# Kernel optimization log

Measured on AMD Instinct MI355X. Metric: run time of the kernel, lower is better.

The kernel has to match this reference:

```python
import jax, jax.numpy as jnp
from jax import lax
import numpy as np

ALPHA = 0.82
MAXITER = 10
N1_NODES = 2048
N2_NODES = 2048
K_ATTR = 64
EDGE_P = 0.004  # sparse-ish adjacency density


def setup_inputs() -> dict:
    key = jax.random.key(0)
    k1, k2, k3, k4 = jax.random.split(key, 4)
    A1 = (jax.random.uniform(k1, (N1_NODES, N1_NODES)) < EDGE_P).astype(jnp.float32)
    A1 = jnp.maximum(A1, A1.T)  # undirected 0/1 adjacency
    A2 = (jax.random.uniform(k2, (N2_NODES, N2_NODES)) < EDGE_P).astype(jnp.float32)
    A2 = jnp.maximum(A2, A2.T)
    N1 = jax.random.uniform(k3, (N1_NODES, K_ATTR), dtype=jnp.float32)
    N2 = jax.random.uniform(k4, (N2_NODES, K_ATTR), dtype=jnp.float32)
    # default prior (_get_H with path=None), normalized so sum ~= 1
    H = jnp.full((N2_NODES, N1_NODES), 1.0 / (N1_NODES * N2_NODES), dtype=jnp.float32)
    return {"A1": A1, "A2": A2, "N1": N1, "N2": N2, "H": H}


def _row_l2_normalize(N):
    nrm = jnp.sqrt(jnp.sum(N * N, axis=1, keepdims=True))
    return jnp.where(nrm > 0, N / jnp.where(nrm > 0, nrm, 1.0), 0.0)


def _final_forward(A1, A2, N1, N2, H, alpha=ALPHA, maxiter=MAXITER):
    # No edge attrs: L=1, E1=A1, E2=A2. T = 1/A^2 where A^2>0 (elementwise),
    # E <- E*T, so B = (E*A) = A*T*A.
    def masked_recip_sq(A):
        A2e = A * A
        return jnp.where(A2e > 0, 1.0 / jnp.where(A2e > 0, A2e, 1.0), 0.0)

    B1 = (A1 * masked_recip_sq(A1)) * A1  # (n1, n1)
    B2 = (A2 * masked_recip_sq(A2)) * A2  # (n2, n2)

    N1n = _row_l2_normalize(N1)  # (n1, K)
    N2n = _row_l2_normalize(N2)  # (n2, K)

    # Kronecker vectors laid out as (n1, n2) matrices (C-order == kron order):
    # N[i*n2+j] = sum_k N1[i,k]*N2[j,k]  -> N1n @ N2n.T
    Nm = N1n @ N2n.T  # (n1, n2)
    dm = (B1 @ N1n) @ (B2 @ N2n).T  # (n1, n2)
    D = Nm * dm
    DD = jnp.where(D > 0, lax.rsqrt(jnp.where(D > 0, D, 1.0)), 0.0)  # inf -> 0
    q = DD * Nm  # (n1, n2)

    # h = H.flatten('F') with H (n2,n1): as an (n1,n2) matrix this is H.T
    h = H.T  # (n1, n2)

    def step(s, _):
        # M = (q*s) reshaped (n2,n1) F-order == (q*s).T in our layout.
        # S = B2 @ M @ B1 (n2,n1); S.flatten('F') as (n1,n2) == B1.T @ (q*s) @ B2.T
        S_t = B1.T @ (q * s) @ B2.T  # (n1, n2)
        s_new = (1.0 - alpha) * h + alpha * q * S_t
        return s_new, None

    s, _ = lax.scan(step, h, None, length=maxiter)
    # original: s.reshape((n1, n2)) C-order -> exactly our layout
    return s  # (n1, n2) alignment matrix


def reference(A1, A2, N1, N2, H):
    return _final_forward(A1, A2, N1, N2, H)
```

## Files before the change

kernel.cpp:

```cpp
#include <hip/hip_runtime.h>

#define NMAT 2048
#define KATTR 64
#define CAP 64
#define NITER 10
#define SENT_A 2048
#define SENT_B 2057

typedef unsigned short ushort4v __attribute__((ext_vector_type(4)));

__device__ __forceinline__ unsigned short f2bf(float f) {
  unsigned u = __float_as_uint(f);
  return (unsigned short)((u + 0x7fff + ((u >> 16) & 1)) >> 16);
}
__device__ __forceinline__ float bf2f(unsigned short b) {
  return __uint_as_float((unsigned)b << 16);
}
__device__ __forceinline__ float bflo(unsigned v) {
  return __uint_as_float(v << 16);
}
__device__ __forceinline__ float bfhi(unsigned v) {
  return __uint_as_float(v & 0xffff0000u);
}
__device__ __forceinline__ int swz(int c) { return 4 * c + (((c >> 3) & 7) << 2); }

__global__ __launch_bounds__(256) void k_build2(
    const float* __restrict__ A1, const float* __restrict__ A2,
    unsigned short* __restrict__ idx1, unsigned short* __restrict__ idx2,
    unsigned short* __restrict__ idxT4, int* __restrict__ cnt1,
    int* __restrict__ cnt2) {
  __shared__ int wsum[4];
  int b = blockIdx.x;
  const float* A;
  unsigned short* idx;
  unsigned short* idxT;
  int* cnt;
  int r;
  if (b < NMAT) {
    A = A1; idx = idx1; idxT = nullptr; cnt = cnt1; r = b;
  } else {
    A = A2; idx = idx2; idxT = idxT4; cnt = cnt2; r = b - NMAT;
  }
  const float* row = A + (size_t)r * NMAT;
  int t = threadIdx.x;
  unsigned mask = 0;
  int ln = 0;
#pragma unroll
  for (int u = 0; u < 8; ++u) {
    int c = t * 8 + u;
    if (row[c] != 0.0f) {
      mask |= 1u << u;
      ++ln;
    }
  }
  int lane = t & 63, wv = t >> 6;
  int v = ln;
  for (int o = 1; o < 64; o <<= 1) {
    int x = __shfl_up(v, o);
    if (lane >= o) v += x;
  }
  if (lane == 63) wsum[wv] = v;
  __syncthreads();
  int base = 0, stot = 0;
#pragma unroll
  for (int w = 0; w < 4; ++w) {
    int x = wsum[w];
    if (w < wv) base += x;
    stot += x;
  }
  int off = base + v - ln;
#pragma unroll
  for (int u = 0; u < 8; ++u) {
    if (mask & (1u << u)) {
      int c = t * 8 + u;
      if (off < CAP) {
        idx[r * CAP + off] = (unsigned short)c;
        if (idxT)
          idxT[(size_t)(off >> 2) * (NMAT * 4) + r * 4 + (off & 3)] =
              (unsigned short)c;
      }
      ++off;
    }
  }
  int n = stot < CAP ? stot : CAP;
  for (int p = n + t; p < CAP; p += 256) {
    idx[r * CAP + p] = (unsigned short)SENT_A;
    if (idxT)
      idxT[(size_t)(p >> 2) * (NMAT * 4) + r * 4 + (p & 3)] =
          (unsigned short)SENT_B;
  }
  if (t == 0) cnt[r] = n;
}

__global__ __launch_bounds__(256) void k_norm2(const float* __restrict__ N1,
                                               const float* __restrict__ N2,
                                               float* __restrict__ N1n,
                                               float* __restrict__ N2n) {
  int half = blockIdx.x >= (NMAT / 4);
  const float* Nin = half ? N2 : N1;
  float* Nout = half ? N2n : N1n;
  int bb = half ? blockIdx.x - NMAT / 4 : blockIdx.x;
  int row = bb * 4 + (threadIdx.x >> 6);
  int lane = threadIdx.x & 63;
  float v = Nin[(size_t)row * KATTR + lane];
  float ss = v * v;
#pragma unroll
  for (int o = 32; o > 0; o >>= 1) ss += __shfl_xor(ss, o);
  float nrm = sqrtf(ss);
  Nout[(size_t)row * KATTR + lane] = (nrm > 0.f) ? v / nrm : 0.f;
}

__global__ void k_gatherN2(const unsigned short* __restrict__ idx1,
                           const int* __restrict__ cnt1,
                           const float* __restrict__ N1n,
                           float* __restrict__ C1,
                           const unsigned short* __restrict__ idx2,
                           const int* __restrict__ cnt2,
                           const float* __restrict__ N2n,
                           float* __restrict__ C2) {
  int half = blockIdx.x >= NMAT;
  const unsigned short* idx = half ? idx2 : idx1;
  const int* cnt = half ? cnt2 : cnt1;
  const float* Nn = half ? N2n : N1n;
  float* C = half ? C2 : C1;
  int i = half ? blockIdx.x - NMAT : blockIdx.x;
  int lane = threadIdx.x;
  int nn = cnt[i];
  const unsigned short* ip = idx + i * CAP;
  float acc = 0.f;
  for (int t = 0; t < nn; ++t) {
    int k = ip[t];
    acc += Nn[(size_t)k * KATTR + lane];
  }
  C[(size_t)i * KATTR + lane] = acc;
}

__global__ __launch_bounds__(1024) void k_zrow(unsigned short* __restrict__ Mb0,
                                               unsigned short* __restrict__ Mb1,
                                               float* __restrict__ Mf) {
  size_t Z = (size_t)NMAT * NMAT;
  for (int o = threadIdx.x; o < NMAT; o += 1024) {
    Mb0[Z + o] = 0;
    Mb1[Z + o] = 0;
    Mf[Z + o] = 0.f;
  }
}

__global__ __launch_bounds__(256) void k_q(
    const float* __restrict__ N1n, const float* __restrict__ C1,
    const float* __restrict__ N2n, const float* __restrict__ C2,
    const float* __restrict__ H, float* __restrict__ q,
    unsigned* __restrict__ QM, unsigned short* __restrict__ M,
    float* __restrict__ Ht) {
  __shared__ float sA[64][68];
  __shared__ float sB[64][68];
  int i0 = blockIdx.y * 64, j0 = blockIdx.x * 64;
  int c = threadIdx.x & 63, r0 = threadIdx.x >> 6;
  int tx = threadIdx.x & 15, ty = threadIdx.x >> 4;
  const float alpha = 0.82f;

  float nmv[4][4] = {};
  float dmv[4][4] = {};

  for (int r = r0; r < 64; r += 4) {
    sA[c][r] = N1n[(size_t)(i0 + r) * KATTR + c];
    sB[c][r] = N2n[(size_t)(j0 + r) * KATTR + c];
  }
  __syncthreads();
#pragma unroll 4
  for (int k = 0; k < 64; ++k) {
    float4 a = *(const float4*)&sA[k][ty * 4];
    float4 b = *(const float4*)&sB[k][tx * 4];
    float av[4] = {a.x, a.y, a.z, a.w};
    float bv[4] = {b.x, b.y, b.z, b.w};
#pragma unroll
    for (int ii = 0; ii < 4; ++ii)
#pragma unroll
      for (int jj = 0; jj < 4; ++jj)
        nmv[ii][jj] = fmaf(av[ii], bv[jj], nmv[ii][jj]);
  }
  __syncthreads();
  for (int r = r0; r < 64; r += 4) {
    sA[c][r] = C1[(size_t)(i0 + r) * KATTR + c];
    sB[c][r] = C2[(size_t)(j0 + r) * KATTR + c];
  }
  __syncthreads();
#pragma unroll 4
  for (int k = 0; k < 64; ++k) {
    float4 a = *(const float4*)&sA[k][ty * 4];
    float4 b = *(const float4*)&sB[k][tx * 4];
    float av[4] = {a.x, a.y, a.z, a.w};
    float bv[4] = {b.x, b.y, b.z, b.w};
#pragma unroll
    for (int ii = 0; ii < 4; ++ii)
#pragma unroll
      for (int jj = 0; jj < 4; ++jj)
        dmv[ii][jj] = fmaf(av[ii], bv[jj], dmv[ii][jj]);
  }
  __syncthreads();
  for (int r = r0; r < 64; r += 4)
    sA[c][r] = H[(size_t)(j0 + r) * NMAT + i0 + c];
  __syncthreads();

#pragma unroll
  for (int ii = 0; ii < 4; ++ii) {
    int i = i0 + ty * 4 + ii;
    size_t base = (size_t)i * NMAT + j0 + tx * 4;
    float4 hv = *(const float4*)&sA[ty * 4 + ii][tx * 4];
    float hvv[4] = {hv.x, hv.y, hv.z, hv.w};
    float qv[4];
    unsigned qmv[4];
    ushort4v mv;
#pragma unroll
    for (int jj = 0; jj < 4; ++jj) {
      float nmx = nmv[ii][jj];
      float D = nmx * dmv[ii][jj];
      float qq = (D > 0.f) ? nmx * rsqrtf(D) : 0.f;
      qv[jj] = qq;
      float m0 = qq * hvv[jj];
      mv[jj] = f2bf(m0);
      qmv[jj] = (unsigned)f2bf(alpha * qq * qq) |
                ((unsigned)f2bf((1.0f - alpha) * m0) << 16);
    }
    *(float4*)&q[base] = make_float4(qv[0], qv[1], qv[2], qv[3]);
    *(uint4*)&QM[base] = make_uint4(qmv[0], qmv[1], qmv[2], qmv[3]);
    *(ushort4v*)&M[base] = mv;
    *(float4*)&Ht[base] = hv;
  }
}

__global__ __launch_bounds__(1024, 8) void k_iter(
    const unsigned short* __restrict__ idx1, const int* __restrict__ cnt1,
    const unsigned short* __restrict__ idx2T4, const int* __restrict__ cnt2,
    const unsigned short* __restrict__ Min, const float* __restrict__ MinF,
    const unsigned* __restrict__ QM, const float* __restrict__ q,
    const float* __restrict__ Ht, unsigned short* __restrict__ Mout,
    float* __restrict__ MoutF, float* __restrict__ sout, int in32, int out32,
    int last) {
  __shared__ float lds[4 * NMAT + 64];
  const int GS = NMAT * 4;
  int i0 = blockIdx.x * 4;
  int tid = threadIdx.x;
  int c0 = tid * 2;

  if (tid == 0) *(float4*)&lds[swz(SENT_B)] = make_float4(0.f, 0.f, 0.f, 0.f);

  float acc[4][2];
#pragma unroll
  for (int r = 0; r < 4; ++r) {
    int nn = cnt1[i0 + r];
    const unsigned short* ip = idx1 + (i0 + r) * CAP;
    uint4 pA = *(const uint4*)(ip);
    uint4 pB = *(const uint4*)(ip + 8);
    uint4 pC = *(const uint4*)(ip + 16);
    uint4 pD = *(const uint4*)(ip + 24);
    float a0 = 0.f, a1 = 0.f;
    if (in32) {
      const float* Bf = MinF + c0;
      auto g8f = [&](uint4 pk, float2* w) {
        w[0] = *(const float2*)(Bf + (size_t)(pk.x & 0xffff) * NMAT);
        w[1] = *(const float2*)(Bf + (size_t)(pk.x >> 16) * NMAT);
        w[2] = *(const float2*)(Bf + (size_t)(pk.y & 0xffff) * NMAT);
        w[3] = *(const float2*)(Bf + (size_t)(pk.y >> 16) * NMAT);
        w[4] = *(const float2*)(Bf + (size_t)(pk.z & 0xffff) * NMAT);
        w[5] = *(const float2*)(Bf + (size_t)(pk.z >> 16) * NMAT);
        w[6] = *(const float2*)(Bf + (size_t)(pk.w & 0xffff) * NMAT);
        w[7] = *(const float2*)(Bf + (size_t)(pk.w >> 16) * NMAT);
      };
      float2 w[16];
      g8f(pA, w);
      g8f(pB, w + 8);
#pragma unroll
      for (int e = 0; e < 16; ++e) {
        a0 += w[e].x;
        a1 += w[e].y;
      }
      if (nn > 16) {
        float2 w2[16];
        g8f(pC, w2);
        g8f(pD, w2 + 8);
#pragma unroll
        for (int e = 0; e < 16; ++e) {
          a0 += w2[e].x;
          a1 += w2[e].y;
        }
      }
      for (int t = 32; t < nn; t += 8) {
        uint4 pk = *(const uint4*)(ip + t);
        float2 w3[8];
        g8f(pk, w3);
#pragma unroll
        for (int e = 0; e < 8; ++e) {
          a0 += w3[e].x;
          a1 += w3[e].y;
        }
      }
    } else {
      const unsigned short* Bb = Min + c0;
      auto g8 = [&](uint4 pk, unsigned* w) {
        w[0] = *(const unsigned*)(Bb + (size_t)(pk.x & 0xffff) * NMAT);
        w[1] = *(const unsigned*)(Bb + (size_t)(pk.x >> 16) * NMAT);
        w[2] = *(const unsigned*)(Bb + (size_t)(pk.y & 0xffff) * NMAT);
        w[3] = *(const unsigned*)(Bb + (size_t)(pk.y >> 16) * NMAT);
        w[4] = *(const unsigned*)(Bb + (size_t)(pk.z & 0xffff) * NMAT);
        w[5] = *(const unsigned*)(Bb + (size_t)(pk.z >> 16) * NMAT);
        w[6] = *(const unsigned*)(Bb + (size_t)(pk.w & 0xffff) * NMAT);
        w[7] = *(const unsigned*)(Bb + (size_t)(pk.w >> 16) * NMAT);
      };
      unsigned w[16];
      g8(pA, w);
      g8(pB, w + 8);
      bool more = nn > 16;
      unsigned w2[16];
      if (more) {
        g8(pC, w2);
        g8(pD, w2 + 8);
      }
#pragma unroll
      for (int e = 0; e < 16; ++e) {
        a0 += bflo(w[e]);
        a1 += bfhi(w[e]);
      }
      if (more) {
#pragma unroll
        for (int e = 0; e < 16; ++e) {
          a0 += bflo(w2[e]);
          a1 += bfhi(w2[e]);
        }
      }
      for (int t = 32; t < nn; t += 8) {
        uint4 pk = *(const uint4*)(ip + t);
        unsigned w3[8];
        g8(pk, w3);
#pragma unroll
        for (int e = 0; e < 8; ++e) {
          a0 += bflo(w3[e]);
          a1 += bfhi(w3[e]);
        }
      }
    }
    acc[r][0] = a0;
    acc[r][1] = a1;
  }
  *(float4*)&lds[swz(c0)] =
      make_float4(acc[0][0], acc[1][0], acc[2][0], acc[3][0]);
  *(float4*)&lds[swz(c0 + 1)] =
      make_float4(acc[0][1], acc[1][1], acc[2][1], acc[3][1]);
  __syncthreads();

  const float alpha = 0.82f;
  const float oma = 1.0f - alpha;
#pragma unroll
  for (int jj = 0; jj < 2; ++jj) {
    int j = jj * 1024 + tid;
    int nn = cnt2[j];
    const unsigned short* bp = idx2T4 + j * 4;
    size_t off0 = (size_t)i0 * NMAT + j;
    unsigned wq0 = 0, wq1 = 0, wq2 = 0, wq3 = 0;
    if (!last) {
      wq0 = QM[off0];
      wq1 = QM[off0 + NMAT];
      wq2 = QM[off0 + 2 * NMAT];
      wq3 = QM[off0 + 3 * NMAT];
    }
    uint2 g0 = *(const uint2*)(bp);
    uint2 g1 = *(const uint2*)(bp + GS);
    uint2 g2 = *(const uint2*)(bp + 2 * GS);
    uint2 g3 = *(const uint2*)(bp + 3 * GS);
    float s0 = 0.f, s1 = 0.f, s2 = 0.f, s3 = 0.f;
    float u0 = 0.f, u1 = 0.f, u2 = 0.f, u3 = 0.f;
    {
      float4 va = *(const float4*)&lds[swz(g0.x & 0xffff)];
      float4 vb = *(const float4*)&lds[swz(g0.x >> 16)];
      float4 vc = *(const float4*)&lds[swz(g0.y & 0xffff)];
      float4 vd = *(const float4*)&lds[swz(g0.y >> 16)];
      float4 ve = *(const float4*)&lds[swz(g1.x & 0xffff)];
      float4 vf = *(const float4*)&lds[swz(g1.x >> 16)];
      float4 vg = *(const float4*)&lds[swz(g1.y & 0xffff)];
      float4 vh = *(const float4*)&lds[swz(g1.y >> 16)];
      s0 += (va.x + vb.x) + (vc.x + vd.x);
      s1 += (va.y + vb.y) + (vc.y + vd.y);
      s2 += (va.z + vb.z) + (vc.z + vd.z);
      s3 += (va.w + vb.w) + (vc.w + vd.w);
      u0 += (ve.x + vf.x) + (vg.x + vh.x);
      u1 += (ve.y + vf.y) + (vg.y + vh.y);
      u2 += (ve.z + vf.z) + (vg.z + vh.z);
      u3 += (ve.w + vf.w) + (vg.w + vh.w);
    }
    {
      float4 va = *(const float4*)&lds[swz(g2.x & 0xffff)];
      float4 vb = *(const float4*)&lds[swz(g2.x >> 16)];
      float4 vc = *(const float4*)&lds[swz(g2.y & 0xffff)];
      float4 vd = *(const float4*)&lds[swz(g2.y >> 16)];
      float4 ve = *(const float4*)&lds[swz(g3.x & 0xffff)];
      float4 vf = *(const float4*)&lds[swz(g3.x >> 16)];
      float4 vg = *(const float4*)&lds[swz(g3.y & 0xffff)];
      float4 vh = *(const float4*)&lds[swz(g3.y >> 16)];
      s0 += (va.x + vb.x) + (vc.x + vd.x);
      s1 += (va.y + vb.y) + (vc.y + vd.y);
      s2 += (va.z + vb.z) + (vc.z + vd.z);
      s3 += (va.w + vb.w) + (vc.w + vd.w);
      u0 += (ve.x + vf.x) + (vg.x + vh.x);
      u1 += (ve.y + vf.y) + (vg.y + vh.y);
      u2 += (ve.z + vf.z) + (vg.z + vh.z);
      u3 += (ve.w + vf.w) + (vg.w + vh.w);
    }
    for (int t = 16; t < nn; t += 8) {
      uint2 ga = *(const uint2*)(bp + (size_t)(t >> 2) * GS);
      uint2 gb = *(const uint2*)(bp + (size_t)((t >> 2) + 1) * GS);
      float4 va = *(const float4*)&lds[swz(ga.x & 0xffff)];
      float4 vb = *(const float4*)&lds[swz(ga.x >> 16)];
      float4 vc = *(const float4*)&lds[swz(ga.y & 0xffff)];
      float4 vd = *(const float4*)&lds[swz(ga.y >> 16)];
      float4 ve = *(const float4*)&lds[swz(gb.x & 0xffff)];
      float4 vf = *(const float4*)&lds[swz(gb.x >> 16)];
      float4 vg = *(const float4*)&lds[swz(gb.y & 0xffff)];
      float4 vh = *(const float4*)&lds[swz(gb.y >> 16)];
      s0 += (va.x + vb.x) + (vc.x + vd.x);
      s1 += (va.y + vb.y) + (vc.y + vd.y);
      s2 += (va.z + vb.z) + (vc.z + vd.z);
      s3 += (va.w + vb.w) + (vc.w + vd.w);
      u0 += (ve.x + vf.x) + (vg.x + vh.x);
      u1 += (ve.y + vf.y) + (vg.y + vh.y);
      u2 += (ve.z + vf.z) + (vg.z + vh.z);
      u3 += (ve.w + vf.w) + (vg.w + vh.w);
    }
    float sa[4] = {s0 + u0, s1 + u1, s2 + u2, s3 + u3};
    if (last) {
#pragma unroll
      for (int r = 0; r < 4; ++r) {
        size_t off = off0 + (size_t)r * NMAT;
        sout[off] = oma * Ht[off] + alpha * q[off] * sa[r];
      }
    } else if (out32) {
      MoutF[off0] = fmaf(bflo(wq0), sa[0], bfhi(wq0));
      MoutF[off0 + NMAT] = fmaf(bflo(wq1), sa[1], bfhi(wq1));
      MoutF[off0 + 2 * NMAT] = fmaf(bflo(wq2), sa[2], bfhi(wq2));
      MoutF[off0 + 3 * NMAT] = fmaf(bflo(wq3), sa[3], bfhi(wq3));
    } else {
      Mout[off0] = f2bf(fmaf(bflo(wq0), sa[0], bfhi(wq0)));
      Mout[off0 + NMAT] = f2bf(fmaf(bflo(wq1), sa[1], bfhi(wq1)));
      Mout[off0 + 2 * NMAT] = f2bf(fmaf(bflo(wq2), sa[2], bfhi(wq2)));
      Mout[off0 + 3 * NMAT] = f2bf(fmaf(bflo(wq3), sa[3], bfhi(wq3)));
    }
  }
}

extern "C" void kernel_launch(void* const* d_in, const int* in_sizes, int n_in,
                              void* d_out, int out_size, void* d_ws,
                              size_t ws_size, hipStream_t stream) {
  const float* A1 = (const float*)d_in[0];
  const float* A2 = (const float*)d_in[1];
  const float* N1 = (const float*)d_in[2];
  const float* N2 = (const float*)d_in[3];
  const float* H = (const float*)d_in[4];
  float* s_out = (float*)d_out;

  char* p = (char*)d_ws;
  auto take = [&](size_t bytes) {
    char* r = p;
    p += (bytes + 255) & ~(size_t)255;
    return r;
  };
  unsigned short* idx1 = (unsigned short*)take((size_t)NMAT * CAP * 2);
  unsigned short* idx2 = (unsigned short*)take((size_t)NMAT * CAP * 2);
  unsigned short* idx2T4 = (unsigned short*)take((size_t)CAP * NMAT * 2);
  int* cnt1 = (int*)take((size_t)NMAT * 4);
  int* cnt2 = (int*)take((size_t)NMAT * 4);
  float* N1n = (float*)take((size_t)NMAT * KATTR * 4);
  float* N2n = (float*)take((size_t)NMAT * KATTR * 4);
  float* C1 = (float*)take((size_t)NMAT * KATTR * 4);
  float* C2 = (float*)take((size_t)NMAT * KATTR * 4);
  float* Ht = (float*)take((size_t)NMAT * NMAT * 4);
  float* q = (float*)take((size_t)NMAT * NMAT * 4);
  unsigned* QM = (unsigned*)take((size_t)NMAT * NMAT * 4);
  unsigned short* Mb0 = (unsigned short*)take((size_t)(NMAT + 1) * NMAT * 2);
  unsigned short* Mb1 = (unsigned short*)take((size_t)(NMAT + 1) * NMAT * 2);
  float* Mf = (float*)take((size_t)(NMAT + 1) * NMAT * 4);
  if ((size_t)(p - (char*)d_ws) > ws_size) return;

  k_build2<<<2 * NMAT, 256, 0, stream>>>(A1, A2, idx1, idx2, idx2T4, cnt1,
                                         cnt2);
  k_norm2<<<2 * (NMAT / 4), 256, 0, stream>>>(N1, N2, N1n, N2n);
  k_gatherN2<<<2 * NMAT, 64, 0, stream>>>(idx1, cnt1, N1n, C1, idx2, cnt2,
                                          N2n, C2);
  k_q<<<dim3(32, 32), 256, 0, stream>>>(N1n, C1, N2n, C2, H, q, QM, Mb0, Ht);
  k_zrow<<<1, 1024, 0, stream>>>(Mb0, Mb1, Mf);
  for (int it = 0; it < NITER; ++it) {
    const unsigned short* Min = (it & 1) ? Mb1 : Mb0;
    unsigned short* Mout = (it & 1) ? Mb0 : Mb1;
    int in32 = (it == NITER - 1) ? 1 : 0;
    int out32 = (it == NITER - 2) ? 1 : 0;
    int last = (it == NITER - 1) ? 1 : 0;
    k_iter<<<NMAT / 4, 1024, 0, stream>>>(idx1, cnt1, idx2T4, cnt2, Min, Mf,
                                          QM, q, Ht, Mout, Mf, s_out, in32,
                                          out32, last);
  }
}
```

Measured before the change: 401.8 us.

## Split iteration kernel into separate B1 and B2 sparse-product phases via fp32 intermediate

Each iteration's fused kernel is split into two launches. Phase A computes the B1 sparse gather for 32-row tiles and 256-column chunks, which gives better cache locality for the gathered rows, and writes the result to a new fp32 scratch matrix. Phase B reloads it into LDS and applies the B2 sparse product and update. This trades the fused on-chip handoff for an extra 16 MB write and read per iteration plus one more launch, in exchange for better reuse in the gather phase.

```diff
diff --git a/kernel.cpp b/kernel.cpp
--- a/kernel.cpp
+++ b/kernel.cpp
@@ -229,34 +229,30 @@
   }
 }
 
-__global__ __launch_bounds__(1024, 8) void k_iter(
+__global__ __launch_bounds__(1024, 8) void k_phA(
     const unsigned short* __restrict__ idx1, const int* __restrict__ cnt1,
-    const unsigned short* __restrict__ idx2T4, const int* __restrict__ cnt2,
     const unsigned short* __restrict__ Min, const float* __restrict__ MinF,
-    const unsigned* __restrict__ QM, const float* __restrict__ q,
-    const float* __restrict__ Ht, unsigned short* __restrict__ Mout,
-    float* __restrict__ MoutF, float* __restrict__ sout, int in32, int out32,
-    int last) {
-  __shared__ float lds[4 * NMAT + 64];
-  const int GS = NMAT * 4;
-  int i0 = blockIdx.x * 4;
+    float* __restrict__ T1, int in32) {
+  int b = blockIdx.x;
+  int chunk = b & 7, tile = b >> 3;
   int tid = threadIdx.x;
-  int c0 = tid * 2;
-
-  if (tid == 0) *(float4*)&lds[swz(SENT_B)] = make_float4(0.f, 0.f, 0.f, 0.f);
-
-  float acc[4][2];
-#pragma unroll
-  for (int r = 0; r < 4; ++r) {
-    int nn = cnt1[i0 + r];
-    const unsigned short* ip = idx1 + (i0 + r) * CAP;
+  int rg = tid >> 7;
+  int l = tid & 127;
+  int jbase = chunk * 256 + l * 2;
+  int irow0 = tile * 32 + rg * 4;
+
+#pragma unroll
+  for (int rr = 0; rr < 4; ++rr) {
+    int i = irow0 + rr;
+    int nn = cnt1[i];
+    const unsigned short* ip = idx1 + i * CAP;
     uint4 pA = *(const uint4*)(ip);
     uint4 pB = *(const uint4*)(ip + 8);
     uint4 pC = *(const uint4*)(ip + 16);
     uint4 pD = *(const uint4*)(ip + 24);
     float a0 = 0.f, a1 = 0.f;
     if (in32) {
-      const float* Bf = MinF + c0;
+      const float* Bf = MinF + jbase;
       auto g8f = [&](uint4 pk, float2* w) {
         w[0] = *(const float2*)(Bf + (size_t)(pk.x & 0xffff) * NMAT);
         w[1] = *(const float2*)(Bf + (size_t)(pk.x >> 16) * NMAT);
@@ -296,7 +292,7 @@
         }
       }
     } else {
-      const unsigned short* Bb = Min + c0;
+      const unsigned short* Bb = Min + jbase;
       auto g8 = [&](uint4 pk, unsigned* w) {
         w[0] = *(const unsigned*)(Bb + (size_t)(pk.x & 0xffff) * NMAT);
         w[1] = *(const unsigned*)(Bb + (size_t)(pk.x >> 16) * NMAT);
@@ -339,13 +335,32 @@
         }
       }
     }
-    acc[r][0] = a0;
-    acc[r][1] = a1;
-  }
-  *(float4*)&lds[swz(c0)] =
-      make_float4(acc[0][0], acc[1][0], acc[2][0], acc[3][0]);
-  *(float4*)&lds[swz(c0 + 1)] =
-      make_float4(acc[0][1], acc[1][1], acc[2][1], acc[3][1]);
+    size_t o = (size_t)i * NMAT + jbase;
+    __builtin_nontemporal_store(a0, T1 + o);
+    __builtin_nontemporal_store(a1, T1 + o + 1);
+  }
+}
+
+__global__ __launch_bounds__(1024, 8) void k_phB(
+    const unsigned short* __restrict__ idx2T4, const int* __restrict__ cnt2,
+    const float* __restrict__ T1, const unsigned* __restrict__ QM,
+    const float* __restrict__ q, const float* __restrict__ Ht,
+    unsigned short* __restrict__ Mout, float* __restrict__ MoutF,
+    float* __restrict__ sout, int out32, int last) {
+  __shared__ float lds[4 * NMAT + 64];
+  const int GS = NMAT * 4;
+  int i0 = blockIdx.x * 4;
+  int tid = threadIdx.x;
+  int c0 = tid * 2;
+
+  if (tid == 0) *(float4*)&lds[swz(SENT_B)] = make_float4(0.f, 0.f, 0.f, 0.f);
+
+  float2 r0 = *(const float2*)&T1[(size_t)(i0 + 0) * NMAT + c0];
+  float2 r1 = *(const float2*)&T1[(size_t)(i0 + 1) * NMAT + c0];
+  float2 r2 = *(const float2*)&T1[(size_t)(i0 + 2) * NMAT + c0];
+  float2 r3 = *(const float2*)&T1[(size_t)(i0 + 3) * NMAT + c0];
+  *(float4*)&lds[swz(c0)] = make_float4(r0.x, r1.x, r2.x, r3.x);
+  *(float4*)&lds[swz(c0 + 1)] = make_float4(r0.y, r1.y, r2.y, r3.y);
   __syncthreads();
 
   const float alpha = 0.82f;
@@ -474,6 +489,7 @@
   float* Ht = (float*)take((size_t)NMAT * NMAT * 4);
   float* q = (float*)take((size_t)NMAT * NMAT * 4);
   unsigned* QM = (unsigned*)take((size_t)NMAT * NMAT * 4);
+  float* T1 = (float*)take((size_t)NMAT * NMAT * 4);
   unsigned short* Mb0 = (unsigned short*)take((size_t)(NMAT + 1) * NMAT * 2);
   unsigned short* Mb1 = (unsigned short*)take((size_t)(NMAT + 1) * NMAT * 2);
   float* Mf = (float*)take((size_t)(NMAT + 1) * NMAT * 4);
@@ -492,8 +508,8 @@
     int in32 = (it == NITER - 1) ? 1 : 0;
     int out32 = (it == NITER - 2) ? 1 : 0;
     int last = (it == NITER - 1) ? 1 : 0;
-    k_iter<<<NMAT / 4, 1024, 0, stream>>>(idx1, cnt1, idx2T4, cnt2, Min, Mf,
-                                          QM, q, Ht, Mout, Mf, s_out, in32,
-                                          out32, last);
-  }
-}
+    k_phA<<<NMAT / 4, 1024, 0, stream>>>(idx1, cnt1, Min, Mf, T1, in32);
+    k_phB<<<NMAT / 4, 1024, 0, stream>>>(idx2T4, cnt2, T1, QM, q, Ht, Mout,
+                                         Mf, s_out, out32, last);
+  }
+}
```

Measured after the change: 562.4 us. 1.4x slower.
